# Kernel optimization log

Hardware: AMD Instinct MI355X
Metric: run time of the kernel (lower is better)

Reference implementation:

```python
import jax, jax.numpy as jnp
import numpy as np

N = 100000      # num vertices
E = 20000       # num hyperedges
NNZ = 600000    # num incidence pairs
D = 128         # feature dim (in_features == out_features)


def _scatter_mean(src, idx, num_segments):
    # mean-reduce rows of src into num_segments buckets; empty buckets -> 0 (matches torch_scatter mean)
    s = jax.ops.segment_sum(src, idx, num_segments=num_segments)
    cnt = jax.ops.segment_sum(jnp.ones((src.shape[0], 1), src.dtype), idx, num_segments=num_segments)
    return s / jnp.maximum(cnt, 1)


def setup_inputs() -> dict:
    key = jax.random.key(0)
    k1, k2, k3, k4, k5 = jax.random.split(key, 5)
    X = jax.random.normal(k1, (N, D), dtype=jnp.float32)
    X0 = jax.random.normal(k2, (N, D), dtype=jnp.float32)
    # nn.Linear weight: [out_features, in_features], kaiming-uniform-ish scale
    W = jax.random.normal(k3, (D, D), dtype=jnp.float32) / np.float32(np.sqrt(D))
    vertex = jax.random.randint(k4, (NNZ,), 0, N)
    edges = jax.random.randint(k5, (NNZ,), 0, E)
    alpha = jnp.float32(0.1)
    beta = jnp.float32(0.5)
    return {"X": X, "vertex": vertex, "edges": edges, "alpha": alpha, "beta": beta, "X0": X0, "W": W}


def reference(X, vertex, edges, alpha, beta, X0, W):
    # vertex -> hyperedge gather + mean
    Xve = X[vertex]                                   # [NNZ, D]
    Xe = _scatter_mean(Xve, edges, E)                 # [E, D]
    # hyperedge -> vertex gather + mean
    Xev = Xe[edges]                                   # [NNZ, D]
    Xv = _scatter_mean(Xev, vertex, N)                # [N, D]
    # GCNII residual mixing (UniGNN_use_norm=False)
    Xi = (1.0 - alpha) * Xv + alpha * X0
    return (1.0 - beta) * Xi + beta * (Xi @ W.T)
```

## Files before the change

kernel.cpp:

```cpp
#include <hip/hip_runtime.h>

#define NV   100000
#define NE   20000
#define NNZP 600000
#define DIM  128
#define SE   80
#define SV   32
#define G_CVT 512

#define NB_E 79
#define NB_V 98
#define CAP_E 8448
#define CAP_V 6912
#define BIN_BLOCKS ((NNZP / 8 + 255) / 256)

typedef __attribute__((ext_vector_type(8))) short short8;
typedef __attribute__((ext_vector_type(4))) float f32x4;

__device__ __forceinline__ unsigned short f2b(float f) {
    unsigned x = __float_as_uint(f);
    unsigned r = x + 0x7fffu + ((x >> 16) & 1u);
    return (unsigned short)(r >> 16);
}
__device__ __forceinline__ float blo(unsigned u) { return __uint_as_float(u << 16); }
__device__ __forceinline__ float bhi(unsigned u) { return __uint_as_float(u & 0xffff0000u); }
__device__ __forceinline__ unsigned pk2(float a, float b) {
    return (unsigned)f2b(a) | ((unsigned)f2b(b) << 16);
}

__global__ __launch_bounds__(256) void k_bin(const float4* __restrict__ X4,
                                             const float4* __restrict__ W4,
                                             const int4* __restrict__ vertex4,
                                             const int4* __restrict__ edges4,
                                             unsigned* __restrict__ gpos_e,
                                             unsigned* __restrict__ gpos_v,
                                             unsigned* __restrict__ ebin,
                                             unsigned* __restrict__ vbin,
                                             ushort4* __restrict__ Xb,
                                             ushort4* __restrict__ Wb) {
    const int b = blockIdx.x;
    if (b < G_CVT) {
        int i = b * 256 + threadIdx.x;
        const int n4 = NV * 32;
        for (int g = i; g < n4; g += G_CVT * 256) {
            float4 v = X4[g];
            ushort4 o; o.x = f2b(v.x); o.y = f2b(v.y); o.z = f2b(v.z); o.w = f2b(v.w);
            Xb[g] = o;
        }
        if (i < DIM * DIM / 4) {
            float4 v = W4[i];
            ushort4 o; o.x = f2b(v.x); o.y = f2b(v.y); o.z = f2b(v.z); o.w = f2b(v.w);
            Wb[i] = o;
        }
        return;
    }

    __shared__ unsigned he[NB_E], hv[NB_V], be[NB_E], bv[NB_V];
    const int tid = threadIdx.x;
    if (tid < NB_E) he[tid] = 0;
    if (tid < NB_V) hv[tid] = 0;
    __syncthreads();

    const int t8 = (b - G_CVT) * 256 + tid;
    const bool ok = t8 < NNZP / 8;
    int vA[8], eA[8];
    unsigned loe[8], lov[8];
    if (ok) {
        int4 v0 = vertex4[t8 * 2], v1 = vertex4[t8 * 2 + 1];
        int4 e0 = edges4[t8 * 2],  e1 = edges4[t8 * 2 + 1];
        vA[0]=v0.x; vA[1]=v0.y; vA[2]=v0.z; vA[3]=v0.w;
        vA[4]=v1.x; vA[5]=v1.y; vA[6]=v1.z; vA[7]=v1.w;
        eA[0]=e0.x; eA[1]=e0.y; eA[2]=e0.z; eA[3]=e0.w;
        eA[4]=e1.x; eA[5]=e1.y; eA[6]=e1.z; eA[7]=e1.w;
#pragma unroll
        for (int k = 0; k < 8; ++k) {
            loe[k] = atomicAdd(&he[eA[k] >> 8], 1u);
            lov[k] = atomicAdd(&hv[vA[k] >> 10], 1u);
        }
    }
    __syncthreads();

    for (int i = tid; i < NB_E; i += 256) {
        int bin = (i + b) % NB_E;
        unsigned h = he[bin];
        be[bin] = h ? atomicAdd(&gpos_e[bin], h) : 0u;
    }
    for (int i = tid; i < NB_V; i += 256) {
        int bin = (i + b) % NB_V;
        unsigned h = hv[bin];
        bv[bin] = h ? atomicAdd(&gpos_v[bin], h) : 0u;
    }
    __syncthreads();

    if (ok) {
#pragma unroll
        for (int k = 0; k < 8; ++k) {
            unsigned e = (unsigned)eA[k], v = (unsigned)vA[k];
            unsigned binE = e >> 8, binV = v >> 10;
            unsigned pe = be[binE] + loe[k];
            if (pe < CAP_E) ebin[(size_t)binE * CAP_E + pe] = (v << 8) | (e & 255u);
            unsigned pv = bv[binV] + lov[k];
            if (pv < CAP_V) vbin[(size_t)binV * CAP_V + pv] = (e << 10) | (v & 1023u);
        }
    }
}

__global__ __launch_bounds__(256) void k_bucket(const unsigned* __restrict__ gpos_e,
                                                const unsigned* __restrict__ gpos_v,
                                                const unsigned* __restrict__ ebin,
                                                const unsigned* __restrict__ vbin,
                                                int* __restrict__ bkt_e,
                                                unsigned short* __restrict__ bkt_v) {
    __shared__ unsigned cl[1024];
    const int tid = threadIdx.x;
    if (blockIdx.x < NB_E) {
        const int b = blockIdx.x;
        cl[tid] = 0;
        __syncthreads();
        unsigned n = gpos_e[b]; if (n > CAP_E) n = CAP_E;
        const unsigned* src = ebin + (size_t)b * CAP_E;
        for (unsigned i = tid; i < n; i += 256) {
            unsigned pk = src[i];
            unsigned el = pk & 255u;
            unsigned slot = atomicAdd(&cl[el], 1u);
            if (slot < SE - 1)
                bkt_e[(size_t)(((unsigned)b << 8) | el) * SE + 1 + slot] = (int)(pk >> 8);
        }
        __syncthreads();
        int e = (b << 8) | tid;
        if (e < NE) bkt_e[(size_t)e * SE] = (int)cl[tid];
    } else {
        const int b = blockIdx.x - NB_E;
        for (int i = tid; i < 1024; i += 256) cl[i] = 0;
        __syncthreads();
        unsigned n = gpos_v[b]; if (n > CAP_V) n = CAP_V;
        const unsigned* src = vbin + (size_t)b * CAP_V;
        for (unsigned i = tid; i < n; i += 256) {
            unsigned pk = src[i];
            unsigned vl = pk & 1023u;
            unsigned slot = atomicAdd(&cl[vl], 1u);
            unsigned v = ((unsigned)b << 10) | vl;
            if (slot < SV - 1)
                bkt_v[(size_t)v * SV + 1 + slot] = (unsigned short)(pk >> 10);
        }
        __syncthreads();
        for (int i = tid; i < 1024; i += 256) {
            int v = (b << 10) + i;
            if (v < NV) bkt_v[(size_t)v * SV] = (unsigned short)cl[i];
        }
    }
}

__global__ __launch_bounds__(256) void k_edge(const uint2* __restrict__ X2,
                                              const int4* __restrict__ bkt4,
                                              uint2* __restrict__ Xeb2) {
    const int t  = blockIdx.x * 256 + threadIdx.x;
    const int e  = t >> 5;
    const int hl = t & 31;
    if (e >= NE) return;
    const int4* bp = bkt4 + (size_t)e * (SE / 4);
    int4 q0 = bp[0], q1 = bp[1], q2 = bp[2], q3 = bp[3], q4 = bp[4], q5 = bp[5],
         q6 = bp[6], q7 = bp[7], q8 = bp[8], q9 = bp[9], q10 = bp[10];
    unsigned c = (unsigned)q0.x; if (c > SE - 1) c = SE - 1;

    float a0 = 0.f, a1 = 0.f, a2 = 0.f, a3 = 0.f;

#define EACC(u_, w_) { a0 += (w_) * blo((u_).x); a1 += (w_) * bhi((u_).x); \
                       a2 += (w_) * blo((u_).y); a3 += (w_) * bhi((u_).y); }
#define EG8(qa, qb, base_) { \
        int id_[8] = {(qa).x, (qa).y, (qa).z, (qa).w, (qb).x, (qb).y, (qb).z, (qb).w}; \
        float wk_[8]; uint2 g_[8]; \
        _Pragma("unroll") \
        for (int k_ = 0; k_ < 8; ++k_) { \
            bool act_ = ((base_) + k_) < c; \
            wk_[k_] = act_ ? 1.0f : 0.0f; \
            g_[k_] = X2[(size_t)(act_ ? (unsigned)id_[k_] : 0u) * 32 + hl]; \
        } \
        _Pragma("unroll") \
        for (int k_ = 0; k_ < 8; ++k_) EACC(g_[k_], wk_[k_]); }

    {
        int id[3] = {q0.y, q0.z, q0.w};
        float wk[3]; uint2 g[3];
#pragma unroll
        for (int k = 0; k < 3; ++k) {
            bool act = (unsigned)k < c;
            wk[k] = act ? 1.0f : 0.0f;
            g[k] = X2[(size_t)(act ? (unsigned)id[k] : 0u) * 32 + hl];
        }
#pragma unroll
        for (int k = 0; k < 3; ++k) EACC(g[k], wk[k]);
    }
    if (c > 3)  EG8(q1, q2, 3u);
    if (c > 11) EG8(q3, q4, 11u);
    if (c > 19) EG8(q5, q6, 19u);
    if (c > 27) EG8(q7, q8, 27u);
    if (c > 35) EG8(q9, q10, 35u);
    for (unsigned j = 43; j < c; j += 8) {
        int4 qa = bp[(j + 1) >> 2];
        int4 qb = bp[((j + 1) >> 2) + 1];
        EG8(qa, qb, j);
    }
#undef EG8
#undef EACC

    const float inv = c ? 1.0f / (float)c : 1.0f;
    uint2 o; o.x = pk2(a0 * inv, a1 * inv); o.y = pk2(a2 * inv, a3 * inv);
    Xeb2[(size_t)e * 32 + hl] = o;
}

__global__ __launch_bounds__(256) void k_vf2(const uint4* __restrict__ Xeb4,
                                             const uint4* __restrict__ bktq,
                                             const float4* __restrict__ X04,
                                             const float* __restrict__ alpha_p,
                                             const float* __restrict__ beta_p,
                                             const unsigned short* __restrict__ Wb,
                                             float* __restrict__ out) {
    __shared__ __align__(16) unsigned sXi[16][68];

    const int tid  = threadIdx.x;
    const int wid  = tid >> 6;
    const int lane = tid & 63;
    const int q    = lane >> 4;
    const int hl   = lane & 15;
    const int vrow = wid * 4 + q;
    const int v    = blockIdx.x * 16 + vrow;

    const float alpha = *alpha_p;

    float4 x0a = X04[(size_t)v * 32 + hl * 2];
    float4 x0b = X04[(size_t)v * 32 + hl * 2 + 1];

    uint4 q0 = bktq[(size_t)v * 4];
    uint4 q1 = bktq[(size_t)v * 4 + 1];
    unsigned c = q0.x & 0xffffu; if (c > SV - 1) c = SV - 1;

    float a[8] = {0.f, 0.f, 0.f, 0.f, 0.f, 0.f, 0.f, 0.f};

#define VACC(g_, w_) { a[0] += (w_) * blo((g_).x); a[1] += (w_) * bhi((g_).x); \
                       a[2] += (w_) * blo((g_).y); a[3] += (w_) * bhi((g_).y); \
                       a[4] += (w_) * blo((g_).z); a[5] += (w_) * bhi((g_).z); \
                       a[6] += (w_) * blo((g_).w); a[7] += (w_) * bhi((g_).w); }

    {
        unsigned id[7] = { q0.x >> 16, q0.y & 0xffffu, q0.y >> 16,
                           q0.z & 0xffffu, q0.z >> 16, q0.w & 0xffffu, q0.w >> 16 };
        float wk[7]; uint4 g[7];
#pragma unroll
        for (int k = 0; k < 7; ++k) {
            bool act = (unsigned)k < c;
            wk[k] = act ? 1.0f : 0.0f;
            g[k] = Xeb4[(size_t)(act ? id[k] : 0u) * 16 + hl];
        }
#pragma unroll
        for (int k = 0; k < 7; ++k) VACC(g[k], wk[k]);
    }
    if (c > 7) {
        unsigned id[8] = { q1.x & 0xffffu, q1.x >> 16, q1.y & 0xffffu, q1.y >> 16,
                           q1.z & 0xffffu, q1.z >> 16, q1.w & 0xffffu, q1.w >> 16 };
        float wk[8]; uint4 g[8];
#pragma unroll
        for (int k = 0; k < 8; ++k) {
            bool act = (unsigned)(7 + k) < c;
            wk[k] = act ? 1.0f : 0.0f;
            g[k] = Xeb4[(size_t)(act ? id[k] : 0u) * 16 + hl];
        }
#pragma unroll
        for (int k = 0; k < 8; ++k) VACC(g[k], wk[k]);
    }
    if (c > 15) {
        uint4 q2 = bktq[(size_t)v * 4 + 2];
        uint4 q3 = bktq[(size_t)v * 4 + 3];
        unsigned id[16] = { q2.x & 0xffffu, q2.x >> 16, q2.y & 0xffffu, q2.y >> 16,
                            q2.z & 0xffffu, q2.z >> 16, q2.w & 0xffffu, q2.w >> 16,
                            q3.x & 0xffffu, q3.x >> 16, q3.y & 0xffffu, q3.y >> 16,
                            q3.z & 0xffffu, q3.z >> 16, q3.w & 0xffffu, q3.w >> 16 };
        float wk[16]; uint4 g[16];
#pragma unroll
        for (int k = 0; k < 16; ++k) {
            bool act = (unsigned)(15 + k) < c;
            wk[k] = act ? 1.0f : 0.0f;
            g[k] = Xeb4[(size_t)(act ? id[k] : 0u) * 16 + hl];
        }
#pragma unroll
        for (int k = 0; k < 16; ++k) VACC(g[k], wk[k]);
    }
#undef VACC

    const float s = (1.0f - alpha) * (c ? 1.0f / (float)c : 1.0f);
    uint4 xiw;
    xiw.x = pk2(s * a[0] + alpha * x0a.x, s * a[1] + alpha * x0a.y);
    xiw.y = pk2(s * a[2] + alpha * x0a.z, s * a[3] + alpha * x0a.w);
    xiw.z = pk2(s * a[4] + alpha * x0b.x, s * a[5] + alpha * x0b.y);
    xiw.w = pk2(s * a[6] + alpha * x0b.z, s * a[7] + alpha * x0b.w);
    *(uint4*)&sXi[vrow][hl * 4] = xiw;
    __syncthreads();

    const float beta = *beta_p;
    const float omb  = 1.0f - beta;
    const int lr = lane & 15;
    const int lg = lane >> 4;

    const char* ab = (const char*)&sXi[lr][0] + lg * 16;
    short8 af[4];
#pragma unroll
    for (int kt = 0; kt < 4; ++kt) af[kt] = *(const short8*)(ab + kt * 64);

#pragma unroll
    for (int ctl = 0; ctl < 2; ++ctl) {
        const int ct = wid * 2 + ctl;
        const unsigned short* Wp = Wb + (size_t)(ct * 16 + lr) * DIM + lg * 8;
        f32x4 acc = {};
#pragma unroll
        for (int kt = 0; kt < 4; ++kt) {
            short8 b = *(const short8*)(Wp + kt * 32);
            acc = __builtin_amdgcn_mfma_f32_16x16x32_bf16(af[kt], b, acc, 0, 0, 0);
        }
#pragma unroll
        for (int rg = 0; rg < 4; ++rg) {
            int row = lg * 4 + rg;
            unsigned u = sXi[row][ct * 8 + (lr >> 1)];
            float xi = (lr & 1) ? bhi(u) : blo(u);
            out[(size_t)(blockIdx.x * 16 + row) * DIM + ct * 16 + lr]
                = omb * xi + beta * acc[rg];
        }
    }
}

extern "C" void kernel_launch(void* const* d_in, const int* in_sizes, int n_in,
                              void* d_out, int out_size, void* d_ws, size_t ws_size,
                              hipStream_t stream) {
    const float* X      = (const float*)d_in[0];
    const int*   vertex = (const int*)  d_in[1];
    const int*   edges  = (const int*)  d_in[2];
    const float* alpha  = (const float*)d_in[3];
    const float* beta   = (const float*)d_in[4];
    const float* X0     = (const float*)d_in[5];
    const float* W      = (const float*)d_in[6];
    float*       out    = (float*)d_out;

    unsigned* gpos_e = (unsigned*)d_ws;
    unsigned* gpos_v = gpos_e + NB_E;
    unsigned* ebin   = (unsigned*)d_ws + 256;
    unsigned* vbin   = ebin + (size_t)NB_E * CAP_E;
    int*      bkt_e  = (int*)(vbin + (size_t)NB_V * CAP_V);
    unsigned short* bkt_v = (unsigned short*)(bkt_e + (size_t)NE * SE);
    unsigned short* Wb = bkt_v + (size_t)NV * SV;
    unsigned* Xeb = (unsigned*)(Wb + DIM * DIM);

    unsigned* Xb = (unsigned*)d_out;

    hipMemsetAsync(d_ws, 0, (size_t)(NB_E + NB_V) * sizeof(unsigned), stream);

    k_bin<<<G_CVT + BIN_BLOCKS, 256, 0, stream>>>(
        (const float4*)X, (const float4*)W, (const int4*)vertex, (const int4*)edges,
        gpos_e, gpos_v, ebin, vbin, (ushort4*)Xb, (ushort4*)Wb);
    k_bucket<<<NB_E + NB_V, 256, 0, stream>>>(gpos_e, gpos_v, ebin, vbin,
                                              bkt_e, bkt_v);
    k_edge<<<(NE * 32 + 255) / 256, 256, 0, stream>>>((const uint2*)Xb,
                                                      (const int4*)bkt_e,
                                                      (uint2*)Xeb);
    k_vf2<<<NV / 16, 256, 0, stream>>>((const uint4*)Xeb, (const uint4*)bkt_v,
                                       (const float4*)X0, alpha, beta, Wb, out);
}
```

Measured before the change: 122.1 us.

## Gather fp32 X directly in edge pass and convert X0 to bf16 there

```diff
diff --git a/kernel.cpp b/kernel.cpp
--- a/kernel.cpp
+++ b/kernel.cpp
@@ -6,13 +6,15 @@
 #define DIM  128
 #define SE   80
 #define SV   32
-#define G_CVT 512
 
 #define NB_E 79
 #define NB_V 98
 #define CAP_E 8448
 #define CAP_V 6912
+#define G_WCVT 16
 #define BIN_BLOCKS ((NNZP / 8 + 255) / 256)
+#define G_CVT0 512
+#define EDGE_BLOCKS (NE * 32 / 256)
 
 typedef __attribute__((ext_vector_type(8))) short short8;
 typedef __attribute__((ext_vector_type(4))) float f32x4;
@@ -28,25 +30,17 @@
     return (unsigned)f2b(a) | ((unsigned)f2b(b) << 16);
 }
 
-__global__ __launch_bounds__(256) void k_bin(const float4* __restrict__ X4,
-                                             const float4* __restrict__ W4,
+__global__ __launch_bounds__(256) void k_bin(const float4* __restrict__ W4,
                                              const int4* __restrict__ vertex4,
                                              const int4* __restrict__ edges4,
                                              unsigned* __restrict__ gpos_e,
                                              unsigned* __restrict__ gpos_v,
                                              unsigned* __restrict__ ebin,
                                              unsigned* __restrict__ vbin,
-                                             ushort4* __restrict__ Xb,
                                              ushort4* __restrict__ Wb) {
     const int b = blockIdx.x;
-    if (b < G_CVT) {
+    if (b < G_WCVT) {
         int i = b * 256 + threadIdx.x;
-        const int n4 = NV * 32;
-        for (int g = i; g < n4; g += G_CVT * 256) {
-            float4 v = X4[g];
-            ushort4 o; o.x = f2b(v.x); o.y = f2b(v.y); o.z = f2b(v.z); o.w = f2b(v.w);
-            Xb[g] = o;
-        }
         if (i < DIM * DIM / 4) {
             float4 v = W4[i];
             ushort4 o; o.x = f2b(v.x); o.y = f2b(v.y); o.z = f2b(v.z); o.w = f2b(v.w);
@@ -61,7 +55,7 @@
     if (tid < NB_V) hv[tid] = 0;
     __syncthreads();
 
-    const int t8 = (b - G_CVT) * 256 + tid;
+    const int t8 = (b - G_WCVT) * 256 + tid;
     const bool ok = t8 < NNZP / 8;
     int vA[8], eA[8];
     unsigned loe[8], lov[8];
@@ -151,13 +145,25 @@
     }
 }
 
-__global__ __launch_bounds__(256) void k_edge(const uint2* __restrict__ X2,
+__global__ __launch_bounds__(256) void k_edge(const float4* __restrict__ X4,
+                                              const float4* __restrict__ X04,
+                                              uint2* __restrict__ X0b2,
                                               const int4* __restrict__ bkt4,
                                               uint2* __restrict__ Xeb2) {
-    const int t  = blockIdx.x * 256 + threadIdx.x;
+    const int bb = blockIdx.x;
+    if (bb < G_CVT0) {
+        int i = bb * 256 + threadIdx.x;
+        const int n4 = NV * 32;
+        for (int g = i; g < n4; g += G_CVT0 * 256) {
+            float4 v = X04[g];
+            uint2 o; o.x = pk2(v.x, v.y); o.y = pk2(v.z, v.w);
+            X0b2[g] = o;
+        }
+        return;
+    }
+    const int t  = (bb - G_CVT0) * 256 + threadIdx.x;
     const int e  = t >> 5;
     const int hl = t & 31;
-    if (e >= NE) return;
     const int4* bp = bkt4 + (size_t)e * (SE / 4);
     int4 q0 = bp[0], q1 = bp[1], q2 = bp[2], q3 = bp[3], q4 = bp[4], q5 = bp[5],
          q6 = bp[6], q7 = bp[7], q8 = bp[8], q9 = bp[9], q10 = bp[10];
@@ -165,28 +171,28 @@
 
     float a0 = 0.f, a1 = 0.f, a2 = 0.f, a3 = 0.f;
 
-#define EACC(u_, w_) { a0 += (w_) * blo((u_).x); a1 += (w_) * bhi((u_).x); \
-                       a2 += (w_) * blo((u_).y); a3 += (w_) * bhi((u_).y); }
+#define EACC(x_, w_) { a0 += (w_) * (x_).x; a1 += (w_) * (x_).y; \
+                       a2 += (w_) * (x_).z; a3 += (w_) * (x_).w; }
 #define EG8(qa, qb, base_) { \
         int id_[8] = {(qa).x, (qa).y, (qa).z, (qa).w, (qb).x, (qb).y, (qb).z, (qb).w}; \
-        float wk_[8]; uint2 g_[8]; \
+        float wk_[8]; float4 g_[8]; \
         _Pragma("unroll") \
         for (int k_ = 0; k_ < 8; ++k_) { \
             bool act_ = ((base_) + k_) < c; \
             wk_[k_] = act_ ? 1.0f : 0.0f; \
-            g_[k_] = X2[(size_t)(act_ ? (unsigned)id_[k_] : 0u) * 32 + hl]; \
+            g_[k_] = X4[(size_t)(act_ ? (unsigned)id_[k_] : 0u) * 32 + hl]; \
         } \
         _Pragma("unroll") \
         for (int k_ = 0; k_ < 8; ++k_) EACC(g_[k_], wk_[k_]); }
 
     {
         int id[3] = {q0.y, q0.z, q0.w};
-        float wk[3]; uint2 g[3];
+        float wk[3]; float4 g[3];
 #pragma unroll
         for (int k = 0; k < 3; ++k) {
             bool act = (unsigned)k < c;
             wk[k] = act ? 1.0f : 0.0f;
-            g[k] = X2[(size_t)(act ? (unsigned)id[k] : 0u) * 32 + hl];
+            g[k] = X4[(size_t)(act ? (unsigned)id[k] : 0u) * 32 + hl];
         }
 #pragma unroll
         for (int k = 0; k < 3; ++k) EACC(g[k], wk[k]);
@@ -211,7 +217,7 @@
 
 __global__ __launch_bounds__(256) void k_vf2(const uint4* __restrict__ Xeb4,
                                              const uint4* __restrict__ bktq,
-                                             const float4* __restrict__ X04,
+                                             const uint4* __restrict__ X0b4,
                                              const float* __restrict__ alpha_p,
                                              const float* __restrict__ beta_p,
                                              const unsigned short* __restrict__ Wb,
@@ -228,8 +234,7 @@
 
     const float alpha = *alpha_p;
 
-    float4 x0a = X04[(size_t)v * 32 + hl * 2];
-    float4 x0b = X04[(size_t)v * 32 + hl * 2 + 1];
+    uint4 x0 = X0b4[(size_t)v * 16 + hl];
 
     uint4 q0 = bktq[(size_t)v * 4];
     uint4 q1 = bktq[(size_t)v * 4 + 1];
@@ -289,10 +294,10 @@
 
     const float s = (1.0f - alpha) * (c ? 1.0f / (float)c : 1.0f);
     uint4 xiw;
-    xiw.x = pk2(s * a[0] + alpha * x0a.x, s * a[1] + alpha * x0a.y);
-    xiw.y = pk2(s * a[2] + alpha * x0a.z, s * a[3] + alpha * x0a.w);
-    xiw.z = pk2(s * a[4] + alpha * x0b.x, s * a[5] + alpha * x0b.y);
-    xiw.w = pk2(s * a[6] + alpha * x0b.z, s * a[7] + alpha * x0b.w);
+    xiw.x = pk2(s * a[0] + alpha * blo(x0.x), s * a[1] + alpha * bhi(x0.x));
+    xiw.y = pk2(s * a[2] + alpha * blo(x0.y), s * a[3] + alpha * bhi(x0.y));
+    xiw.z = pk2(s * a[4] + alpha * blo(x0.z), s * a[5] + alpha * bhi(x0.z));
+    xiw.w = pk2(s * a[6] + alpha * blo(x0.w), s * a[7] + alpha * bhi(x0.w));
     *(uint4*)&sXi[vrow][hl * 4] = xiw;
     __syncthreads();
 
@@ -347,19 +352,18 @@
     unsigned short* bkt_v = (unsigned short*)(bkt_e + (size_t)NE * SE);
     unsigned short* Wb = bkt_v + (size_t)NV * SV;
     unsigned* Xeb = (unsigned*)(Wb + DIM * DIM);
-
-    unsigned* Xb = (unsigned*)d_out;
+    unsigned* X0b = Xeb + (size_t)NE * 64;
 
     hipMemsetAsync(d_ws, 0, (size_t)(NB_E + NB_V) * sizeof(unsigned), stream);
 
-    k_bin<<<G_CVT + BIN_BLOCKS, 256, 0, stream>>>(
-        (const float4*)X, (const float4*)W, (const int4*)vertex, (const int4*)edges,
-        gpos_e, gpos_v, ebin, vbin, (ushort4*)Xb, (ushort4*)Wb);
+    k_bin<<<G_WCVT + BIN_BLOCKS, 256, 0, stream>>>(
+        (const float4*)W, (const int4*)vertex, (const int4*)edges,
+        gpos_e, gpos_v, ebin, vbin, (ushort4*)Wb);
     k_bucket<<<NB_E + NB_V, 256, 0, stream>>>(gpos_e, gpos_v, ebin, vbin,
                                               bkt_e, bkt_v);
-    k_edge<<<(NE * 32 + 255) / 256, 256, 0, stream>>>((const uint2*)Xb,
-                                                      (const int4*)bkt_e,
-                                                      (uint2*)Xeb);
+    k_edge<<<G_CVT0 + EDGE_BLOCKS, 256, 0, stream>>>(
+        (const float4*)X, (const float4*)X0, (uint2*)X0b,
+        (const int4*)bkt_e, (uint2*)Xeb);
     k_vf2<<<NV / 16, 256, 0, stream>>>((const uint4*)Xeb, (const uint4*)bkt_v,
-                                       (const float4*)X0, alpha, beta, Wb, out);
-}
+                                       (const uint4*)X0b, alpha, beta, Wb, out);
+}
```

Result: slower. 144.8 us (+18.6%).

## Split X bf16 conversion across bin and bucket kernels to overlap work

Applied to the files above, without the earlier changes.

```diff
diff --git a/kernel.cpp b/kernel.cpp
--- a/kernel.cpp
+++ b/kernel.cpp
@@ -6,13 +6,16 @@
 #define DIM  128
 #define SE   80
 #define SV   32
-#define G_CVT 512
 
 #define NB_E 79
 #define NB_V 98
 #define CAP_E 8448
 #define CAP_V 6912
 #define BIN_BLOCKS ((NNZP / 8 + 255) / 256)
+#define G_CVT1 256
+#define G_CVT2 384
+#define XSPLIT4 1280000
+#define EDGE_BLOCKS (NE * 32 / 256)
 
 typedef __attribute__((ext_vector_type(8))) short short8;
 typedef __attribute__((ext_vector_type(4))) float f32x4;
@@ -39,10 +42,9 @@
                                              ushort4* __restrict__ Xb,
                                              ushort4* __restrict__ Wb) {
     const int b = blockIdx.x;
-    if (b < G_CVT) {
-        int i = b * 256 + threadIdx.x;
-        const int n4 = NV * 32;
-        for (int g = i; g < n4; g += G_CVT * 256) {
+    if (b >= BIN_BLOCKS) {
+        int i = (b - BIN_BLOCKS) * 256 + threadIdx.x;
+        for (int g = i; g < XSPLIT4; g += G_CVT1 * 256) {
             float4 v = X4[g];
             ushort4 o; o.x = f2b(v.x); o.y = f2b(v.y); o.z = f2b(v.z); o.w = f2b(v.w);
             Xb[g] = o;
@@ -61,7 +63,7 @@
     if (tid < NB_V) hv[tid] = 0;
     __syncthreads();
 
-    const int t8 = (b - G_CVT) * 256 + tid;
+    const int t8 = b * 256 + tid;
     const bool ok = t8 < NNZP / 8;
     int vA[8], eA[8];
     unsigned loe[8], lov[8];
@@ -110,9 +112,22 @@
                                                 const unsigned* __restrict__ ebin,
                                                 const unsigned* __restrict__ vbin,
                                                 int* __restrict__ bkt_e,
-                                                unsigned short* __restrict__ bkt_v) {
+                                                unsigned short* __restrict__ bkt_v,
+                                                const float4* __restrict__ X4,
+                                                ushort4* __restrict__ Xb) {
+    const int tid = threadIdx.x;
+    if (blockIdx.x >= NB_E + NB_V) {
+        int i = (blockIdx.x - NB_E - NB_V) * 256 + tid;
+        const int n4 = NV * 32;
+        for (int g = XSPLIT4 + i; g < n4; g += G_CVT2 * 256) {
+            float4 v = X4[g];
+            ushort4 o; o.x = f2b(v.x); o.y = f2b(v.y); o.z = f2b(v.z); o.w = f2b(v.w);
+            Xb[g] = o;
+        }
+        return;
+    }
+
     __shared__ unsigned cl[1024];
-    const int tid = threadIdx.x;
     if (blockIdx.x < NB_E) {
         const int b = blockIdx.x;
         cl[tid] = 0;
@@ -352,14 +367,15 @@
 
     hipMemsetAsync(d_ws, 0, (size_t)(NB_E + NB_V) * sizeof(unsigned), stream);
 
-    k_bin<<<G_CVT + BIN_BLOCKS, 256, 0, stream>>>(
+    k_bin<<<BIN_BLOCKS + G_CVT1, 256, 0, stream>>>(
         (const float4*)X, (const float4*)W, (const int4*)vertex, (const int4*)edges,
         gpos_e, gpos_v, ebin, vbin, (ushort4*)Xb, (ushort4*)Wb);
-    k_bucket<<<NB_E + NB_V, 256, 0, stream>>>(gpos_e, gpos_v, ebin, vbin,
-                                              bkt_e, bkt_v);
-    k_edge<<<(NE * 32 + 255) / 256, 256, 0, stream>>>((const uint2*)Xb,
-                                                      (const int4*)bkt_e,
-                                                      (uint2*)Xeb);
+    k_bucket<<<NB_E + NB_V + G_CVT2, 256, 0, stream>>>(
+        gpos_e, gpos_v, ebin, vbin, bkt_e, bkt_v,
+        (const float4*)X, (ushort4*)Xb);
+    k_edge<<<EDGE_BLOCKS, 256, 0, stream>>>((const uint2*)Xb,
+                                            (const int4*)bkt_e,
+                                            (uint2*)Xeb);
     k_vf2<<<NV / 16, 256, 0, stream>>>((const uint4*)Xeb, (const uint4*)bkt_v,
                                        (const float4*)X0, alpha, beta, Wb, out);
 }
```

Result: no change. 122.3 us (+0.1%).
